# Kernel tuning notes

Measured on AMD Instinct MI355X. Metric: run time of the kernel, lower is better.

## Reference

```python
import jax, jax.numpy as jnp
import numpy as np

THRESHOLD = 1.0

@jax.custom_vjp
def spike(u):
    # Heaviside fire with snntorch ATan surrogate gradient (alpha=2.0)
    return (u > 0).astype(u.dtype)

def _spike_fwd(u):
    return spike(u), u

def _spike_bwd(u, g):
    # d/du atan surrogate: (alpha/2) / (1 + (pi/2*alpha*u)^2) with alpha=2 -> 1/(1+(pi*u)^2)
    return (g / (1.0 + (jnp.pi * u) ** 2),)

spike.defvjp(_spike_fwd, _spike_bwd)


def setup_inputs() -> dict:
    key = jax.random.key(0)
    k1, k2, k3, k4 = jax.random.split(key, 4)
    B, D, M = 1024, 256, 256
    x = jax.random.normal(k1, (B, D), dtype=jnp.float32)
    mem_states = jax.random.normal(k2, (M, B, D), dtype=jnp.float32)
    # mode_selector Linear(D -> M)
    W = jax.random.normal(k3, (M, D), dtype=jnp.float32) / np.sqrt(D)
    b = jax.random.normal(k4, (M,), dtype=jnp.float32) * 0.01
    return {"x": x, "mem_states": mem_states, "W": W, "b": b}


def reference(x, mem_states, W, b):
    M = mem_states.shape[0]
    # gating scores: [B, M]
    mode_scores = jax.nn.softmax(x @ W.T + b, axis=-1)
    # snn.Leaky(beta=i) for i in range(M): beta is the integer loop index
    betas = jnp.arange(M, dtype=x.dtype)[:, None, None]  # [M,1,1]
    # subtract-reset uses detached spike of the incoming membrane
    reset = jax.lax.stop_gradient((mem_states - THRESHOLD > 0).astype(x.dtype))
    mem_new = betas * mem_states + x[None, :, :] - reset * THRESHOLD  # [M,B,D]
    spk = spike(mem_new - THRESHOLD)  # [M,B,D]
    # faithful to source broadcast: [M,B,D] * [1,B,M] (requires D == M), sum over modes
    mixed = (spk * mode_scores[None, :, :]).sum(axis=0)  # [B,D]
    return mixed, mem_new, mode_scores
```

## Files before the change

### kernel.cpp

```cpp
#include <hip/hip_runtime.h>

#define THRESH 1.0f

typedef float fvec4 __attribute__((ext_vector_type(4)));

__global__ __launch_bounds__(256) void transpose_kernel(
    const float* __restrict__ W, float* __restrict__ Wt, int M, int D)
{
    __shared__ float tile[32][33];
    const int tilesK = D / 32;
    const int bx = blockIdx.x % tilesK;
    const int by = blockIdx.x / tilesK;
    const int lx = threadIdx.x & 31;
    const int ly = threadIdx.x >> 5;
    #pragma unroll
    for (int j = 0; j < 4; ++j)
        tile[ly + j * 8][lx] = W[(size_t)(by * 32 + ly + j * 8) * D + bx * 32 + lx];
    __syncthreads();
    #pragma unroll
    for (int j = 0; j < 4; ++j)
        Wt[(size_t)(bx * 32 + ly + j * 8) * M + by * 32 + lx] = tile[lx][ly + j * 8];
}

__global__ __launch_bounds__(256) void scores_kernel2(
    const float* __restrict__ Wt, const float* __restrict__ x,
    const float* __restrict__ bias, float* __restrict__ scores,
    int D, int M)
{
    const int b   = blockIdx.x;
    const int tid = threadIdx.x;
    const int wave = tid >> 6;
    const int lane = tid & 63;
    __shared__ __align__(16) float x_lds[256];
    __shared__ float wred[4];

    x_lds[tid] = x[(size_t)b * D + tid];
    __syncthreads();

    float a0 = 0.f, a1 = 0.f, a2 = 0.f, a3 = 0.f;
    const float4* x4l = reinterpret_cast<const float4*>(x_lds);
    #pragma unroll 4
    for (int k = 0; k < D; k += 4) {
        const float4 xk = x4l[k >> 2];
        a0 = fmaf(Wt[(size_t)(k + 0) * M + tid], xk.x, a0);
        a1 = fmaf(Wt[(size_t)(k + 1) * M + tid], xk.y, a1);
        a2 = fmaf(Wt[(size_t)(k + 2) * M + tid], xk.z, a2);
        a3 = fmaf(Wt[(size_t)(k + 3) * M + tid], xk.w, a3);
    }
    const float l = (a0 + a1) + (a2 + a3) + bias[tid];

    float mx = l;
    #pragma unroll
    for (int off = 32; off; off >>= 1) mx = fmaxf(mx, __shfl_xor(mx, off, 64));
    if (lane == 0) wred[wave] = mx;
    __syncthreads();
    mx = fmaxf(fmaxf(wred[0], wred[1]), fmaxf(wred[2], wred[3]));
    __syncthreads();

    const float e = expf(l - mx);
    float s = e;
    #pragma unroll
    for (int off = 32; off; off >>= 1) s += __shfl_xor(s, off, 64);
    if (lane == 0) wred[wave] = s;
    __syncthreads();
    const float tot = wred[0] + wred[1] + wred[2] + wred[3];

    scores[(size_t)b * M + tid] = e / tot;
}

__global__ __launch_bounds__(256) void neuron_count_kernel(
    const float* __restrict__ x, const float* __restrict__ mem,
    float* __restrict__ mem_new, float* __restrict__ counts,
    int plane4, int nPosBlocks, int mchunk)
{
    const int posb = blockIdx.x % nPosBlocks;
    const int mc   = blockIdx.x / nPosBlocks;
    const int idx  = posb * 256 + threadIdx.x;
    if (idx >= plane4) return;

    const fvec4* x4   = reinterpret_cast<const fvec4*>(x);
    const fvec4* mem4 = reinterpret_cast<const fvec4*>(mem);
    fvec4* out4       = reinterpret_cast<fvec4*>(mem_new);

    const fvec4 xv = x4[idx];
    const int m0 = mc * mchunk;
    float cx = 0.f, cy = 0.f, cz = 0.f, cw = 0.f;

    #pragma unroll 4
    for (int mm = 0; mm < mchunk; ++mm) {
        const int m = m0 + mm;
        const float bm = (float)m;
        const size_t off = (size_t)m * plane4 + idx;
        const fvec4 mv = __builtin_nontemporal_load(&mem4[off]);

        fvec4 nv;
        nv.x = __fsub_rn(__fadd_rn(__fmul_rn(bm, mv.x), xv.x),
                         (mv.x - THRESH > 0.f) ? THRESH : 0.f);
        nv.y = __fsub_rn(__fadd_rn(__fmul_rn(bm, mv.y), xv.y),
                         (mv.y - THRESH > 0.f) ? THRESH : 0.f);
        nv.z = __fsub_rn(__fadd_rn(__fmul_rn(bm, mv.z), xv.z),
                         (mv.z - THRESH > 0.f) ? THRESH : 0.f);
        nv.w = __fsub_rn(__fadd_rn(__fmul_rn(bm, mv.w), xv.w),
                         (mv.w - THRESH > 0.f) ? THRESH : 0.f);

        __builtin_nontemporal_store(nv, &out4[off]);

        cx += (nv.x - THRESH > 0.f) ? 1.f : 0.f;
        cy += (nv.y - THRESH > 0.f) ? 1.f : 0.f;
        cz += (nv.z - THRESH > 0.f) ? 1.f : 0.f;
        cw += (nv.w - THRESH > 0.f) ? 1.f : 0.f;
    }
    fvec4 cv; cv.x = cx; cv.y = cy; cv.z = cz; cv.w = cw;
    reinterpret_cast<fvec4*>(counts)[(size_t)mc * plane4 + idx] = cv;
}

__global__ __launch_bounds__(256) void mix_kernel(
    const float* __restrict__ scores, const float* __restrict__ counts,
    float* __restrict__ mixed, int plane4, int nchunk)
{
    const int idx = blockIdx.x * 256 + threadIdx.x;
    if (idx >= plane4) return;
    const fvec4* c4 = reinterpret_cast<const fvec4*>(counts);
    fvec4 c = c4[idx];
    for (int j = 1; j < nchunk; ++j) {
        const fvec4 cj = c4[(size_t)j * plane4 + idx];
        c.x += cj.x; c.y += cj.y; c.z += cj.z; c.w += cj.w;
    }
    const fvec4 sc = reinterpret_cast<const fvec4*>(scores)[idx];
    fvec4 mx;
    mx.x = sc.x * c.x; mx.y = sc.y * c.y; mx.z = sc.z * c.z; mx.w = sc.w * c.w;
    reinterpret_cast<fvec4*>(mixed)[idx] = mx;
}

__global__ __launch_bounds__(256) void scores_kernel_fb(
    const float* __restrict__ x, const float* __restrict__ W,
    const float* __restrict__ bias, float* __restrict__ scores,
    int D, int M)
{
    const int b = blockIdx.x;
    __shared__ __align__(16) float x_lds[256];
    __shared__ float logits[256];
    __shared__ float wred[4];
    const int tid  = threadIdx.x;
    const int wave = tid >> 6;
    const int lane = tid & 63;
    x_lds[tid] = x[(size_t)b * D + tid];
    __syncthreads();
    const float4* W4 = reinterpret_cast<const float4*>(W);
    const float4  xv = reinterpret_cast<const float4*>(x_lds)[lane];
    for (int i = 0; i < 64; ++i) {
        const int m = wave * 64 + i;
        const float4 wv = W4[(size_t)m * 64 + lane];
        float p = wv.x * xv.x + wv.y * xv.y + wv.z * xv.z + wv.w * xv.w;
        #pragma unroll
        for (int off = 32; off; off >>= 1) p += __shfl_xor(p, off, 64);
        if (lane == 0) logits[m] = p + bias[m];
    }
    __syncthreads();
    float l = logits[tid];
    float mx = l;
    #pragma unroll
    for (int off = 32; off; off >>= 1) mx = fmaxf(mx, __shfl_xor(mx, off, 64));
    if (lane == 0) wred[wave] = mx;
    __syncthreads();
    mx = fmaxf(fmaxf(wred[0], wred[1]), fmaxf(wred[2], wred[3]));
    __syncthreads();
    const float e = expf(l - mx);
    float s = e;
    #pragma unroll
    for (int off = 32; off; off >>= 1) s += __shfl_xor(s, off, 64);
    if (lane == 0) wred[wave] = s;
    __syncthreads();
    const float tot = wred[0] + wred[1] + wred[2] + wred[3];
    scores[(size_t)b * M + tid] = e / tot;
}

__global__ __launch_bounds__(256) void neuron_kernel_fb(
    const float* __restrict__ x, const float* __restrict__ mem,
    const float* __restrict__ scores, float* __restrict__ mixed,
    float* __restrict__ mem_new, int M, int plane4)
{
    const int idx = blockIdx.x * 256 + threadIdx.x;
    if (idx >= plane4) return;
    const float4* x4   = reinterpret_cast<const float4*>(x);
    const float4* mem4 = reinterpret_cast<const float4*>(mem);
    const float4* sc4  = reinterpret_cast<const float4*>(scores);
    float4* out4       = reinterpret_cast<float4*>(mem_new);
    float4* mix4       = reinterpret_cast<float4*>(mixed);
    const float4 xv = x4[idx];
    float cx = 0.f, cy = 0.f, cz = 0.f, cw = 0.f;
    #pragma unroll 4
    for (int m = 0; m < M; ++m) {
        const float bm = (float)m;
        const size_t off = (size_t)m * plane4 + idx;
        const float4 mv = mem4[off];
        float4 nv;
        nv.x = __fsub_rn(__fadd_rn(__fmul_rn(bm, mv.x), xv.x),
                         (mv.x - THRESH > 0.f) ? THRESH : 0.f);
        nv.y = __fsub_rn(__fadd_rn(__fmul_rn(bm, mv.y), xv.y),
                         (mv.y - THRESH > 0.f) ? THRESH : 0.f);
        nv.z = __fsub_rn(__fadd_rn(__fmul_rn(bm, mv.z), xv.z),
                         (mv.z - THRESH > 0.f) ? THRESH : 0.f);
        nv.w = __fsub_rn(__fadd_rn(__fmul_rn(bm, mv.w), xv.w),
                         (mv.w - THRESH > 0.f) ? THRESH : 0.f);
        out4[off] = nv;
        cx += (nv.x - THRESH > 0.f) ? 1.f : 0.f;
        cy += (nv.y - THRESH > 0.f) ? 1.f : 0.f;
        cz += (nv.z - THRESH > 0.f) ? 1.f : 0.f;
        cw += (nv.w - THRESH > 0.f) ? 1.f : 0.f;
    }
    const float4 sc = sc4[idx];
    float4 mx;
    mx.x = sc.x * cx; mx.y = sc.y * cy; mx.z = sc.z * cz; mx.w = sc.w * cw;
    mix4[idx] = mx;
}

extern "C" void kernel_launch(void* const* d_in, const int* in_sizes, int n_in,
                              void* d_out, int out_size, void* d_ws, size_t ws_size,
                              hipStream_t stream) {
    const float* x    = (const float*)d_in[0];
    const float* mem  = (const float*)d_in[1];
    const float* W    = (const float*)d_in[2];
    const float* bias = (const float*)d_in[3];

    const int M = in_sizes[3];
    const int D = in_sizes[2] / M;
    const int B = in_sizes[0] / D;
    const int plane  = B * D;
    const int plane4 = plane / 4;

    float* out_mixed  = (float*)d_out;
    float* out_mem    = out_mixed + plane;
    float* out_scores = out_mem + (size_t)M * plane;

    const int nchunk = 4;
    const int mchunk = M / nchunk;
    const size_t wt_bytes    = (size_t)M * D * sizeof(float);
    const size_t count_bytes = (size_t)nchunk * plane4 * 16;

    if (ws_size >= wt_bytes + count_bytes) {
        float* Wt     = (float*)d_ws;
        float* counts = (float*)((char*)d_ws + wt_bytes);

        transpose_kernel<<<(M / 32) * (D / 32), 256, 0, stream>>>(W, Wt, M, D);
        scores_kernel2<<<B, 256, 0, stream>>>(Wt, x, bias, out_scores, D, M);

        const int nPosBlocks = (plane4 + 255) / 256;
        neuron_count_kernel<<<nPosBlocks * nchunk, 256, 0, stream>>>(
            x, mem, out_mem, counts, plane4, nPosBlocks, mchunk);
        mix_kernel<<<nPosBlocks, 256, 0, stream>>>(
            out_scores, counts, out_mixed, plane4, nchunk);
    } else {
        scores_kernel_fb<<<B, 256, 0, stream>>>(x, W, bias, out_scores, D, M);
        neuron_kernel_fb<<<(plane4 + 255) / 256, 256, 0, stream>>>(
            x, mem, out_scores, out_mixed, out_mem, M, plane4);
    }
}
```

Measured before the change: 116.5 us.

## Batch four rows per scores block and prefetch eight mem planes per iteration

The scores kernel now handles four batch rows per block, so each Wt load is reused across four dot products and the softmax reductions run four-wide. The neuron kernel issues eight independent nontemporal loads before computing, to raise memory-level parallelism. The mix kernel reads counts with nontemporal loads. A shape guard sends other sizes to the fallback path, and the scores grid shrinks to B/4 blocks, which lowers occupancy for that kernel.

```diff
diff --git a/kernel.cpp b/kernel.cpp
--- a/kernel.cpp
+++ b/kernel.cpp
@@ -22,50 +22,85 @@
         Wt[(size_t)(bx * 32 + ly + j * 8) * M + by * 32 + lx] = tile[lx][ly + j * 8];
 }
 
-__global__ __launch_bounds__(256) void scores_kernel2(
+__global__ __launch_bounds__(256) void scores_kernel4(
     const float* __restrict__ Wt, const float* __restrict__ x,
     const float* __restrict__ bias, float* __restrict__ scores,
     int D, int M)
 {
-    const int b   = blockIdx.x;
-    const int tid = threadIdx.x;
+    const int b0   = blockIdx.x * 4;
+    const int tid  = threadIdx.x;
     const int wave = tid >> 6;
     const int lane = tid & 63;
-    __shared__ __align__(16) float x_lds[256];
-    __shared__ float wred[4];
-
-    x_lds[tid] = x[(size_t)b * D + tid];
+    __shared__ __align__(16) float x_lds[4][256];
+    __shared__ float wredm[4][4];
+    __shared__ float wreds[4][4];
+
+    #pragma unroll
+    for (int r = 0; r < 4; ++r)
+        x_lds[r][tid] = x[(size_t)(b0 + r) * D + tid];
     __syncthreads();
 
     float a0 = 0.f, a1 = 0.f, a2 = 0.f, a3 = 0.f;
-    const float4* x4l = reinterpret_cast<const float4*>(x_lds);
-    #pragma unroll 4
-    for (int k = 0; k < D; k += 4) {
-        const float4 xk = x4l[k >> 2];
-        a0 = fmaf(Wt[(size_t)(k + 0) * M + tid], xk.x, a0);
-        a1 = fmaf(Wt[(size_t)(k + 1) * M + tid], xk.y, a1);
-        a2 = fmaf(Wt[(size_t)(k + 2) * M + tid], xk.z, a2);
-        a3 = fmaf(Wt[(size_t)(k + 3) * M + tid], xk.w, a3);
-    }
-    const float l = (a0 + a1) + (a2 + a3) + bias[tid];
-
-    float mx = l;
-    #pragma unroll
-    for (int off = 32; off; off >>= 1) mx = fmaxf(mx, __shfl_xor(mx, off, 64));
-    if (lane == 0) wred[wave] = mx;
-    __syncthreads();
-    mx = fmaxf(fmaxf(wred[0], wred[1]), fmaxf(wred[2], wred[3]));
-    __syncthreads();
-
-    const float e = expf(l - mx);
-    float s = e;
-    #pragma unroll
-    for (int off = 32; off; off >>= 1) s += __shfl_xor(s, off, 64);
-    if (lane == 0) wred[wave] = s;
-    __syncthreads();
-    const float tot = wred[0] + wred[1] + wred[2] + wred[3];
-
-    scores[(size_t)b * M + tid] = e / tot;
+    #pragma unroll 2
+    for (int k4 = 0; k4 < D / 4; ++k4) {
+        const fvec4 x0 = reinterpret_cast<const fvec4*>(x_lds[0])[k4];
+        const fvec4 x1 = reinterpret_cast<const fvec4*>(x_lds[1])[k4];
+        const fvec4 x2 = reinterpret_cast<const fvec4*>(x_lds[2])[k4];
+        const fvec4 x3 = reinterpret_cast<const fvec4*>(x_lds[3])[k4];
+        #pragma unroll
+        for (int j = 0; j < 4; ++j) {
+            const float w = Wt[(size_t)(k4 * 4 + j) * M + tid];
+            a0 = fmaf(w, x0[j], a0);
+            a1 = fmaf(w, x1[j], a1);
+            a2 = fmaf(w, x2[j], a2);
+            a3 = fmaf(w, x3[j], a3);
+        }
+    }
+    const float bv = bias[tid];
+    float l0 = a0 + bv, l1 = a1 + bv, l2 = a2 + bv, l3 = a3 + bv;
+
+    float m0 = l0, m1 = l1, m2 = l2, m3 = l3;
+    #pragma unroll
+    for (int off = 32; off; off >>= 1) {
+        m0 = fmaxf(m0, __shfl_xor(m0, off, 64));
+        m1 = fmaxf(m1, __shfl_xor(m1, off, 64));
+        m2 = fmaxf(m2, __shfl_xor(m2, off, 64));
+        m3 = fmaxf(m3, __shfl_xor(m3, off, 64));
+    }
+    if (lane == 0) {
+        wredm[0][wave] = m0; wredm[1][wave] = m1;
+        wredm[2][wave] = m2; wredm[3][wave] = m3;
+    }
+    __syncthreads();
+    m0 = fmaxf(fmaxf(wredm[0][0], wredm[0][1]), fmaxf(wredm[0][2], wredm[0][3]));
+    m1 = fmaxf(fmaxf(wredm[1][0], wredm[1][1]), fmaxf(wredm[1][2], wredm[1][3]));
+    m2 = fmaxf(fmaxf(wredm[2][0], wredm[2][1]), fmaxf(wredm[2][2], wredm[2][3]));
+    m3 = fmaxf(fmaxf(wredm[3][0], wredm[3][1]), fmaxf(wredm[3][2], wredm[3][3]));
+
+    const float e0 = expf(l0 - m0), e1 = expf(l1 - m1);
+    const float e2 = expf(l2 - m2), e3 = expf(l3 - m3);
+    float s0 = e0, s1 = e1, s2 = e2, s3 = e3;
+    #pragma unroll
+    for (int off = 32; off; off >>= 1) {
+        s0 += __shfl_xor(s0, off, 64);
+        s1 += __shfl_xor(s1, off, 64);
+        s2 += __shfl_xor(s2, off, 64);
+        s3 += __shfl_xor(s3, off, 64);
+    }
+    if (lane == 0) {
+        wreds[0][wave] = s0; wreds[1][wave] = s1;
+        wreds[2][wave] = s2; wreds[3][wave] = s3;
+    }
+    __syncthreads();
+    const float t0 = wreds[0][0] + wreds[0][1] + wreds[0][2] + wreds[0][3];
+    const float t1 = wreds[1][0] + wreds[1][1] + wreds[1][2] + wreds[1][3];
+    const float t2 = wreds[2][0] + wreds[2][1] + wreds[2][2] + wreds[2][3];
+    const float t3 = wreds[3][0] + wreds[3][1] + wreds[3][2] + wreds[3][3];
+
+    scores[(size_t)(b0 + 0) * M + tid] = e0 / t0;
+    scores[(size_t)(b0 + 1) * M + tid] = e1 / t1;
+    scores[(size_t)(b0 + 2) * M + tid] = e2 / t2;
+    scores[(size_t)(b0 + 3) * M + tid] = e3 / t3;
 }
 
 __global__ __launch_bounds__(256) void neuron_count_kernel(
@@ -86,29 +121,34 @@
     const int m0 = mc * mchunk;
     float cx = 0.f, cy = 0.f, cz = 0.f, cw = 0.f;
 
-    #pragma unroll 4
-    for (int mm = 0; mm < mchunk; ++mm) {
-        const int m = m0 + mm;
-        const float bm = (float)m;
-        const size_t off = (size_t)m * plane4 + idx;
-        const fvec4 mv = __builtin_nontemporal_load(&mem4[off]);
-
-        fvec4 nv;
-        nv.x = __fsub_rn(__fadd_rn(__fmul_rn(bm, mv.x), xv.x),
-                         (mv.x - THRESH > 0.f) ? THRESH : 0.f);
-        nv.y = __fsub_rn(__fadd_rn(__fmul_rn(bm, mv.y), xv.y),
-                         (mv.y - THRESH > 0.f) ? THRESH : 0.f);
-        nv.z = __fsub_rn(__fadd_rn(__fmul_rn(bm, mv.z), xv.z),
-                         (mv.z - THRESH > 0.f) ? THRESH : 0.f);
-        nv.w = __fsub_rn(__fadd_rn(__fmul_rn(bm, mv.w), xv.w),
-                         (mv.w - THRESH > 0.f) ? THRESH : 0.f);
-
-        __builtin_nontemporal_store(nv, &out4[off]);
-
-        cx += (nv.x - THRESH > 0.f) ? 1.f : 0.f;
-        cy += (nv.y - THRESH > 0.f) ? 1.f : 0.f;
-        cz += (nv.z - THRESH > 0.f) ? 1.f : 0.f;
-        cw += (nv.w - THRESH > 0.f) ? 1.f : 0.f;
+    for (int mm = 0; mm < mchunk; mm += 8) {
+        fvec4 mv[8];
+        #pragma unroll
+        for (int j = 0; j < 8; ++j)
+            mv[j] = __builtin_nontemporal_load(
+                &mem4[(size_t)(m0 + mm + j) * plane4 + idx]);
+
+        #pragma unroll
+        for (int j = 0; j < 8; ++j) {
+            const float bm = (float)(m0 + mm + j);
+            fvec4 nv;
+            nv.x = __fsub_rn(__fadd_rn(__fmul_rn(bm, mv[j].x), xv.x),
+                             (mv[j].x - THRESH > 0.f) ? THRESH : 0.f);
+            nv.y = __fsub_rn(__fadd_rn(__fmul_rn(bm, mv[j].y), xv.y),
+                             (mv[j].y - THRESH > 0.f) ? THRESH : 0.f);
+            nv.z = __fsub_rn(__fadd_rn(__fmul_rn(bm, mv[j].z), xv.z),
+                             (mv[j].z - THRESH > 0.f) ? THRESH : 0.f);
+            nv.w = __fsub_rn(__fadd_rn(__fmul_rn(bm, mv[j].w), xv.w),
+                             (mv[j].w - THRESH > 0.f) ? THRESH : 0.f);
+
+            __builtin_nontemporal_store(nv,
+                &out4[(size_t)(m0 + mm + j) * plane4 + idx]);
+
+            cx += (nv.x - THRESH > 0.f) ? 1.f : 0.f;
+            cy += (nv.y - THRESH > 0.f) ? 1.f : 0.f;
+            cz += (nv.z - THRESH > 0.f) ? 1.f : 0.f;
+            cw += (nv.w - THRESH > 0.f) ? 1.f : 0.f;
+        }
     }
     fvec4 cv; cv.x = cx; cv.y = cy; cv.z = cz; cv.w = cw;
     reinterpret_cast<fvec4*>(counts)[(size_t)mc * plane4 + idx] = cv;
@@ -121,9 +161,9 @@
     const int idx = blockIdx.x * 256 + threadIdx.x;
     if (idx >= plane4) return;
     const fvec4* c4 = reinterpret_cast<const fvec4*>(counts);
-    fvec4 c = c4[idx];
+    fvec4 c = __builtin_nontemporal_load(&c4[idx]);
     for (int j = 1; j < nchunk; ++j) {
-        const fvec4 cj = c4[(size_t)j * plane4 + idx];
+        const fvec4 cj = __builtin_nontemporal_load(&c4[(size_t)j * plane4 + idx]);
         c.x += cj.x; c.y += cj.y; c.z += cj.z; c.w += cj.w;
     }
     const fvec4 sc = reinterpret_cast<const fvec4*>(scores)[idx];
@@ -238,12 +278,15 @@
     const size_t wt_bytes    = (size_t)M * D * sizeof(float);
     const size_t count_bytes = (size_t)nchunk * plane4 * 16;
 
-    if (ws_size >= wt_bytes + count_bytes) {
+    const bool shapes_ok = (B % 4 == 0) && (D == 256) && (M == 256) &&
+                           (mchunk % 8 == 0);
+
+    if (shapes_ok && ws_size >= wt_bytes + count_bytes) {
         float* Wt     = (float*)d_ws;
         float* counts = (float*)((char*)d_ws + wt_bytes);
 
         transpose_kernel<<<(M / 32) * (D / 32), 256, 0, stream>>>(W, Wt, M, D);
-        scores_kernel2<<<B, 256, 0, stream>>>(Wt, x, bias, out_scores, D, M);
+        scores_kernel4<<<B / 4, 256, 0, stream>>>(Wt, x, bias, out_scores, D, M);
 
         const int nPosBlocks = (plane4 + 255) / 256;
         neuron_count_kernel<<<nPosBlocks * nchunk, 256, 0, stream>>>(
```

After: 137.3 us. 1.18x slower.
